# Kernel optimization log

Measured on AMD Instinct MI355X. Metric: run time of the kernel, lower is better.

The kernel has to match this reference:

```python
import jax, jax.numpy as jnp
import numpy as np

GRID = 7
COORD = 5.0
NO_OBJ = 0.5


def _corners(xywh, r, c):
    # xywh: [...,4] with (x_cell, y_cell, w, h); r,c broadcastable grid indices
    x, y, w, h = xywh[..., 0], xywh[..., 1], xywh[..., 2], xywh[..., 3]
    cx = (x + c) / GRID
    cy = (y + r) / GRID
    return cx - w / 2, cy - h / 2, cx + w / 2, cy + h / 2


def _iou(a, b):
    ax1, ay1, ax2, ay2 = a
    bx1, by1, bx2, by2 = b
    iw = jnp.maximum(jnp.minimum(ax2, bx2) - jnp.maximum(ax1, bx1), 0.0)
    ih = jnp.maximum(jnp.minimum(ay2, by2) - jnp.maximum(ay1, by1), 0.0)
    inter = iw * ih
    area_a = (ax2 - ax1) * (ay2 - ay1)
    area_b = (bx2 - bx1) * (by2 - by1)
    union = area_a + area_b - inter
    return jnp.where(union > 0, inter / jnp.where(union > 0, union, 1.0), 0.0)


def setup_inputs() -> dict:
    key = jax.random.key(0)
    k1, k2, k3 = jax.random.split(key, 3)
    B = 8192
    data = jax.random.uniform(k1, (B, GRID, GRID, 30), dtype=jnp.float32)
    labels = jax.random.uniform(k2, (B, GRID, GRID, 30), dtype=jnp.float32)
    # obj flag at channel 4 must be exactly 1 for obj cells
    obj = jax.random.randint(k3, (B, GRID, GRID), 0, 2).astype(jnp.float32)
    labels = labels.at[..., 4].set(obj)
    return {"data": data, "labels": labels}


def reference(data, labels):
    B = data.shape[0]
    r = jnp.arange(GRID, dtype=data.dtype)[None, :, None]  # row index -> y offset
    c = jnp.arange(GRID, dtype=data.dtype)[None, None, :]  # col index -> x offset

    box1 = _corners(data[..., 0:4], r, c)
    box2 = _corners(data[..., 5:9], r, c)
    gt = _corners(labels[..., 0:4], r, c)

    iou1 = _iou(box1, gt)  # [B,7,7]
    iou2 = _iou(box2, gt)
    resp1 = iou1 >= iou2

    xy1 = jnp.sum((data[..., 0:2] - labels[..., 0:2]) ** 2, -1)
    xy2 = jnp.sum((data[..., 5:7] - labels[..., 5:7]) ** 2, -1)
    wh1 = jnp.sum((jnp.sqrt(data[..., 2:4]) - jnp.sqrt(labels[..., 2:4])) ** 2, -1)
    wh2 = jnp.sum((jnp.sqrt(data[..., 7:9]) - jnp.sqrt(labels[..., 7:9])) ** 2, -1)

    d4, d9 = data[..., 4], data[..., 9]
    co = COORD * jnp.where(resp1, xy1, xy2)
    wh = COORD * jnp.where(resp1, wh1, wh2)
    confi = jnp.where(resp1, (d4 - iou1) ** 2, (d9 - iou2) ** 2)
    noobj_in = NO_OBJ * jnp.where(resp1, d9 ** 2, d4 ** 2)
    cls = jnp.sum((data[..., 10:] - labels[..., 10:]) ** 2, -1)

    m = (labels[..., 4] == 1).astype(data.dtype)
    obj_loss = m * (co + wh + confi + noobj_in + cls)
    noobj_loss = (1.0 - m) * NO_OBJ * (d4 ** 2 + d9 ** 2)
    return jnp.sum(obj_loss + noobj_loss) / B
```

## Files before the change

kernel.cpp:

```cpp
#include <hip/hip_runtime.h>

#define COORD 5.0f
#define NO_OBJ 0.5f
#define NCELLS (8192 * 49)
#define INV_B (1.0f / 8192.0f)

#define CPB 64
#define FPT (CPB * 30)
#define NTILES (NCELLS / CPB)
#define NPBLK 1280

__device__ __forceinline__ float iou_calc(float ax1, float ay1, float ax2, float ay2,
                                          float bx1, float by1, float bx2, float by2) {
    float iw = fminf(ax2, bx2) - fmaxf(ax1, bx1);
    iw = fmaxf(iw, 0.0f);
    float ih = fminf(ay2, by2) - fmaxf(ay1, by1);
    ih = fmaxf(ih, 0.0f);
    float inter = iw * ih;
    float area_a = (ax2 - ax1) * (ay2 - ay1);
    float area_b = (bx2 - bx1) * (by2 - by1);
    float uni = area_a + area_b - inter;
    return uni > 0.0f ? inter / uni : 0.0f;
}

__device__ __forceinline__ void stage_tile(const float* __restrict__ g, float* s, int tid) {
#pragma unroll
    for (int j = 0; j < 7; j++) {
        __builtin_amdgcn_global_load_lds(
            (const __attribute__((address_space(1))) void*)(g + j * 256 + tid * 4),
            (__attribute__((address_space(3))) void*)(s + j * 256 + tid * 4), 16, 0, 0);
    }
#pragma unroll
    for (int j = 0; j < 2; j++) {
        __builtin_amdgcn_global_load_lds(
            (const __attribute__((address_space(1))) void*)(g + 1792 + j * 64 + tid),
            (__attribute__((address_space(3))) void*)(s + 1792 + j * 64 + tid), 4, 0, 0);
    }
}

__device__ __forceinline__ float cell_loss(const float* __restrict__ sd,
                                           const float* __restrict__ sl,
                                           int idx, int tid) {
    const int cell = idx % 49;
    const float r = (float)(cell / 7);
    const float c = (float)(cell % 7);

    float d[30], l[30];
    const float2* dp = (const float2*)(sd + tid * 30);
    const float2* lp = (const float2*)(sl + tid * 30);
#pragma unroll
    for (int i = 0; i < 15; i++) {
        float2 v = dp[i];
        d[2 * i] = v.x; d[2 * i + 1] = v.y;
        float2 w2 = lp[i];
        l[2 * i] = w2.x; l[2 * i + 1] = w2.y;
    }

    const float inv_g = 1.0f / 7.0f;
    float cx1 = (d[0] + c) * inv_g, cy1 = (d[1] + r) * inv_g;
    float b1x1 = cx1 - d[2] * 0.5f, b1y1 = cy1 - d[3] * 0.5f;
    float b1x2 = cx1 + d[2] * 0.5f, b1y2 = cy1 + d[3] * 0.5f;
    float cx2 = (d[5] + c) * inv_g, cy2 = (d[6] + r) * inv_g;
    float b2x1 = cx2 - d[7] * 0.5f, b2y1 = cy2 - d[8] * 0.5f;
    float b2x2 = cx2 + d[7] * 0.5f, b2y2 = cy2 + d[8] * 0.5f;
    float gx = (l[0] + c) * inv_g, gy = (l[1] + r) * inv_g;
    float gx1 = gx - l[2] * 0.5f, gy1 = gy - l[3] * 0.5f;
    float gx2 = gx + l[2] * 0.5f, gy2 = gy + l[3] * 0.5f;

    float iou1 = iou_calc(b1x1, b1y1, b1x2, b1y2, gx1, gy1, gx2, gy2);
    float iou2 = iou_calc(b2x1, b2y1, b2x2, b2y2, gx1, gy1, gx2, gy2);
    bool resp1 = iou1 >= iou2;

    float xy1 = (d[0] - l[0]) * (d[0] - l[0]) + (d[1] - l[1]) * (d[1] - l[1]);
    float xy2 = (d[5] - l[5]) * (d[5] - l[5]) + (d[6] - l[6]) * (d[6] - l[6]);
    float s2 = sqrtf(d[2]) - sqrtf(l[2]);
    float s3 = sqrtf(d[3]) - sqrtf(l[3]);
    float wh1 = s2 * s2 + s3 * s3;
    float s7 = sqrtf(d[7]) - sqrtf(l[7]);
    float s8 = sqrtf(d[8]) - sqrtf(l[8]);
    float wh2 = s7 * s7 + s8 * s8;

    float d4 = d[4], d9 = d[9];
    float co = COORD * (resp1 ? xy1 : xy2);
    float wh = COORD * (resp1 ? wh1 : wh2);
    float ci = resp1 ? (d4 - iou1) * (d4 - iou1) : (d9 - iou2) * (d9 - iou2);
    float noobj_in = NO_OBJ * (resp1 ? d9 * d9 : d4 * d4);
    float cls = 0.0f;
#pragma unroll
    for (int i = 10; i < 30; i++) {
        float t = d[i] - l[i];
        cls += t * t;
    }

    return (l[4] == 1.0f) ? (co + wh + ci + noobj_in + cls)
                          : NO_OBJ * (d4 * d4 + d9 * d9);
}

__global__ __launch_bounds__(CPB) void yolo_loss_kernel(
    const float* __restrict__ data, const float* __restrict__ labels,
    float* __restrict__ ws) {
    __shared__ float sd[2][FPT];
    __shared__ float sl[2][FPT];

    const int tid = threadIdx.x;
    const int bid = blockIdx.x;
    const int n = (NTILES - bid + NPBLK - 1) / NPBLK;

    stage_tile(data + (size_t)bid * FPT, sd[0], tid);
    stage_tile(labels + (size_t)bid * FPT, sl[0], tid);
    if (n > 1) {
        const size_t t1 = (size_t)(bid + NPBLK) * FPT;
        stage_tile(data + t1, sd[1], tid);
        stage_tile(labels + t1, sl[1], tid);
    }

    float acc = 0.0f;
    for (int i = 0; i < n; ++i) {
        const int cur = i & 1;
        if (i + 1 < n) {
            asm volatile("s_waitcnt vmcnt(18)" ::: "memory");
        } else {
            asm volatile("s_waitcnt vmcnt(0)" ::: "memory");
        }
        acc += cell_loss(sd[cur], sl[cur], (bid + i * NPBLK) * CPB + tid, tid);
        if (i + 2 < n) {
            asm volatile("s_waitcnt lgkmcnt(0)" ::: "memory");
            const size_t t2 = (size_t)(bid + (i + 2) * NPBLK) * FPT;
            stage_tile(data + t2, sd[cur], tid);
            stage_tile(labels + t2, sl[cur], tid);
        }
    }
    acc *= INV_B;

#pragma unroll
    for (int off = 32; off > 0; off >>= 1)
        acc += __shfl_down(acc, off, 64);
    if (tid == 0) ws[bid] = acc;
}

__global__ __launch_bounds__(256) void reduce_kernel(const float* __restrict__ ws,
                                                     float* __restrict__ out) {
    float s = 0.0f;
    for (int i = threadIdx.x; i < NPBLK; i += 256) s += ws[i];
#pragma unroll
    for (int off = 32; off > 0; off >>= 1)
        s += __shfl_down(s, off, 64);
    __shared__ float w[4];
    if ((threadIdx.x & 63) == 0) w[threadIdx.x >> 6] = s;
    __syncthreads();
    if (threadIdx.x == 0) out[0] = w[0] + w[1] + w[2] + w[3];
}

extern "C" void kernel_launch(void* const* d_in, const int* in_sizes, int n_in,
                              void* d_out, int out_size, void* d_ws, size_t ws_size,
                              hipStream_t stream) {
    const float* data = (const float*)d_in[0];
    const float* labels = (const float*)d_in[1];
    float* out = (float*)d_out;
    float* ws = (float*)d_ws;

    yolo_loss_kernel<<<NPBLK, CPB, 0, stream>>>(data, labels, ws);
    reduce_kernel<<<1, 256, 0, stream>>>(ws, out);
}
```

Before: 111.2 us.

## Fuse final reduction via cooperative grid sync and use contiguous tile ranges per block

Replaces the separate reduce kernel with a cooperative-launch grid sync inside the main kernel, so block 0 sums the per-block partials and one launch is removed. Each block now processes a contiguous run of 4 or 5 tiles instead of tiles strided by the grid size, which changes the memory access locality. Grid sync adds a barrier cost and requires all 1280 blocks to be co-resident.

Result: slower. 321.2 us (+188.9%).

```diff
diff --git a/kernel.cpp b/kernel.cpp
--- a/kernel.cpp
+++ b/kernel.cpp
@@ -1,4 +1,7 @@
 #include <hip/hip_runtime.h>
+#include <hip/hip_cooperative_groups.h>
+
+namespace cg = cooperative_groups;
 
 #define COORD 5.0f
 #define NO_OBJ 0.5f
@@ -9,6 +12,8 @@
 #define FPT (CPB * 30)
 #define NTILES (NCELLS / CPB)
 #define NPBLK 1280
+#define QT 4
+#define RT 1152
 
 __device__ __forceinline__ float iou_calc(float ax1, float ay1, float ax2, float ay2,
                                           float bx1, float by1, float bx2, float by2) {
@@ -98,21 +103,19 @@
 
 __global__ __launch_bounds__(CPB) void yolo_loss_kernel(
     const float* __restrict__ data, const float* __restrict__ labels,
-    float* __restrict__ ws) {
+    float* __restrict__ ws, float* __restrict__ out) {
     __shared__ float sd[2][FPT];
     __shared__ float sl[2][FPT];
 
     const int tid = threadIdx.x;
     const int bid = blockIdx.x;
-    const int n = (NTILES - bid + NPBLK - 1) / NPBLK;
+    const int n = QT + (bid < RT ? 1 : 0);
+    const int start = bid * QT + (bid < RT ? bid : RT);
 
-    stage_tile(data + (size_t)bid * FPT, sd[0], tid);
-    stage_tile(labels + (size_t)bid * FPT, sl[0], tid);
-    if (n > 1) {
-        const size_t t1 = (size_t)(bid + NPBLK) * FPT;
-        stage_tile(data + t1, sd[1], tid);
-        stage_tile(labels + t1, sl[1], tid);
-    }
+    stage_tile(data + (size_t)start * FPT, sd[0], tid);
+    stage_tile(labels + (size_t)start * FPT, sl[0], tid);
+    stage_tile(data + (size_t)(start + 1) * FPT, sd[1], tid);
+    stage_tile(labels + (size_t)(start + 1) * FPT, sl[1], tid);
 
     float acc = 0.0f;
     for (int i = 0; i < n; ++i) {
@@ -122,12 +125,11 @@
         } else {
             asm volatile("s_waitcnt vmcnt(0)" ::: "memory");
         }
-        acc += cell_loss(sd[cur], sl[cur], (bid + i * NPBLK) * CPB + tid, tid);
+        acc += cell_loss(sd[cur], sl[cur], (start + i) * CPB + tid, tid);
         if (i + 2 < n) {
             asm volatile("s_waitcnt lgkmcnt(0)" ::: "memory");
-            const size_t t2 = (size_t)(bid + (i + 2) * NPBLK) * FPT;
-            stage_tile(data + t2, sd[cur], tid);
-            stage_tile(labels + t2, sl[cur], tid);
+            stage_tile(data + (size_t)(start + i + 2) * FPT, sd[cur], tid);
+            stage_tile(labels + (size_t)(start + i + 2) * FPT, sl[cur], tid);
         }
     }
     acc *= INV_B;
@@ -136,19 +138,18 @@
     for (int off = 32; off > 0; off >>= 1)
         acc += __shfl_down(acc, off, 64);
     if (tid == 0) ws[bid] = acc;
-}
 
-__global__ __launch_bounds__(256) void reduce_kernel(const float* __restrict__ ws,
-                                                     float* __restrict__ out) {
-    float s = 0.0f;
-    for (int i = threadIdx.x; i < NPBLK; i += 256) s += ws[i];
+    __threadfence();
+    cg::this_grid().sync();
+
+    if (bid == 0) {
+        float s = 0.0f;
+        for (int i = tid; i < NPBLK; i += CPB) s += ws[i];
 #pragma unroll
-    for (int off = 32; off > 0; off >>= 1)
-        s += __shfl_down(s, off, 64);
-    __shared__ float w[4];
-    if ((threadIdx.x & 63) == 0) w[threadIdx.x >> 6] = s;
-    __syncthreads();
-    if (threadIdx.x == 0) out[0] = w[0] + w[1] + w[2] + w[3];
+        for (int off = 32; off > 0; off >>= 1)
+            s += __shfl_down(s, off, 64);
+        if (tid == 0) out[0] = s;
+    }
 }
 
 extern "C" void kernel_launch(void* const* d_in, const int* in_sizes, int n_in,
@@ -159,6 +160,7 @@
     float* out = (float*)d_out;
     float* ws = (float*)d_ws;
 
-    yolo_loss_kernel<<<NPBLK, CPB, 0, stream>>>(data, labels, ws);
-    reduce_kernel<<<1, 256, 0, stream>>>(ws, out);
+    void* args[] = {(void*)&data, (void*)&labels, (void*)&ws, (void*)&out};
+    hipLaunchCooperativeKernel((const void*)yolo_loss_kernel, dim3(NPBLK), dim3(CPB),
+                               args, 0, stream);
 }
```
